# Optimization experiments

Measured on AMD Instinct MI355X. Metric: run time of the kernel, lower is better.

The kernel has to match this reference:

```python
import jax, jax.numpy as jnp
import numpy as np

V, H, L = 32000, 512, 1
B, S = 16, 64


def setup_inputs() -> dict:
    key = jax.random.key(0)
    ks = jax.random.split(key, 10)
    inp = {
        "target_seqs": jax.random.randint(ks[0], (B, S), 0, V),
        "thought": jax.random.normal(ks[1], (1, B, H), dtype=jnp.float32),
        "hidden": jax.random.normal(ks[2], (L, B, H), dtype=jnp.float32),
        # parameters
        "emb": jax.random.normal(ks[3], (V, H), dtype=jnp.float32) * 0.02,
        "W_ih": jax.random.normal(ks[4], (3 * H, 2 * H), dtype=jnp.float32) * (1.0 / np.sqrt(H)),
        "W_hh": jax.random.normal(ks[5], (3 * H, H), dtype=jnp.float32) * (1.0 / np.sqrt(H)),
        "b_ih": jax.random.normal(ks[6], (3 * H,), dtype=jnp.float32) * 0.01,
        "b_hh": jax.random.normal(ks[7], (3 * H,), dtype=jnp.float32) * 0.01,
        "W_out": jax.random.normal(ks[8], (V, H), dtype=jnp.float32) * (1.0 / np.sqrt(H)),
        "b_out": jax.random.normal(ks[9], (V,), dtype=jnp.float32) * 0.01,
    }
    return inp


def gru_layer(x_sbd, h0, W_ih, W_hh, b_ih, b_hh):
    # x_sbd: [S,B,2H]; h0: [B,H]. Torch GRU cell math.
    # Precompute input projections for all timesteps: [S,B,3H]
    gi = jnp.einsum('sbd,gd->sbg', x_sbd, W_ih) + b_ih

    def step(h, gi_t):
        gh = h @ W_hh.T + b_hh                       # [B,3H]
        i_r, i_z, i_n = jnp.split(gi_t, 3, axis=-1)
        h_r, h_z, h_n = jnp.split(gh, 3, axis=-1)
        r = jax.nn.sigmoid(i_r + h_r)
        z = jax.nn.sigmoid(i_z + h_z)
        n = jnp.tanh(i_n + r * h_n)
        h_new = (1.0 - z) * n + z * h
        return h_new, h_new

    h_last, ys = jax.lax.scan(step, h0, gi)
    return ys, h_last                                 # [S,B,H], [B,H]


def reference(target_seqs, thought, hidden, emb, W_ih, W_hh, b_ih, b_hh, W_out, b_out):
    embedded = emb[target_seqs]                        # [B,S,H]
    # fused broadcast-concat replacing the python double loop
    th = jnp.broadcast_to(thought[0][:, None, :], embedded.shape)  # [B,S,H]
    rnn_input = jnp.concatenate([embedded, th], axis=-1)           # [B,S,2H]
    x_sbd = jnp.transpose(rnn_input, (1, 0, 2))                    # [S,B,2H]
    ys, h_last = gru_layer(x_sbd, hidden[0], W_ih, W_hh, b_ih, b_hh)
    output = jnp.transpose(ys, (1, 0, 2))              # [B,S,H]
    logits = jnp.einsum('bsh,vh->bsv', output, W_out) + b_out
    logp = jax.nn.log_softmax(logits, axis=-1)         # [B,S,V]
    return logp, h_last[None]                          # hidden: [1,B,H]
```

## Files before the change

### kernel.cpp

```cpp
#include <hip/hip_runtime.h>

typedef unsigned int u32;
typedef unsigned short u16;
typedef short s16x8 __attribute__((ext_vector_type(8)));
typedef float f32x4 __attribute__((ext_vector_type(4)));

#define SENT 0xFFFFFFFFu

__device__ __forceinline__ u16 f2bf(float f) {
  u32 u = __float_as_uint(f);
  u32 r = (u + 0x7fffu + ((u >> 16) & 1u)) >> 16;
  return (u16)r;
}

__device__ __forceinline__ uint4 load_u4_bypass(const u32* p) {
  uint4 r;
  asm volatile("global_load_dwordx4 %0, %1, off sc0 sc1\n\ts_waitcnt vmcnt(0)"
               : "=v"(r) : "v"(p) : "memory");
  return r;
}

__device__ __forceinline__ void gload16(const u16* g, u16* l) {
  __builtin_amdgcn_global_load_lds(
      (const __attribute__((address_space(1))) unsigned int*)(g),
      (__attribute__((address_space(3))) unsigned int*)(l), 16, 0, 0);
}

__global__ __launch_bounds__(256) void cvt_bf16_kernel(const float* __restrict__ src,
                                                       u16* __restrict__ dst, int n4) {
  int i = blockIdx.x * 256 + threadIdx.x;
  if (i >= n4) return;
  float4 v = reinterpret_cast<const float4*>(src)[i];
  u32 lo = (u32)f2bf(v.x) | ((u32)f2bf(v.y) << 16);
  u32 hi = (u32)f2bf(v.z) | ((u32)f2bf(v.w) << 16);
  reinterpret_cast<uint2*>(dst)[i] = make_uint2(lo, hi);
}

__global__ __launch_bounds__(128) void build_x_kernel(const int* __restrict__ tseq,
                                                      const float* __restrict__ emb,
                                                      const float* __restrict__ thought,
                                                      u16* __restrict__ x) {
  int m = blockIdx.x;
  int s = m >> 4, b = m & 15;
  int tid = threadIdx.x;
  int k = tid * 8;
  const float* src;
  if (k < 512) src = emb + (size_t)tseq[b * 64 + s] * 512 + k;
  else         src = thought + b * 512 + (k - 512);
  float4 v0 = reinterpret_cast<const float4*>(src)[0];
  float4 v1 = reinterpret_cast<const float4*>(src)[1];
  uint4 o;
  o.x = (u32)f2bf(v0.x) | ((u32)f2bf(v0.y) << 16);
  o.y = (u32)f2bf(v0.z) | ((u32)f2bf(v0.w) << 16);
  o.z = (u32)f2bf(v1.x) | ((u32)f2bf(v1.y) << 16);
  o.w = (u32)f2bf(v1.z) | ((u32)f2bf(v1.w) << 16);
  *reinterpret_cast<uint4*>(x + (size_t)m * 1024 + k) = o;
}

template <bool LSE>
__global__ __launch_bounds__(256) void gemm_bt_kernel(const u16* __restrict__ A,
                                                      const u16* __restrict__ Bm,
                                                      const float* __restrict__ bias,
                                                      float* __restrict__ C,
                                                      int M_, int N_, int K_,
                                                      float* __restrict__ partials, int nnb) {
  __shared__ u16 sA[2][4096];
  __shared__ u16 sB[2][4096];
  __shared__ float pm[2][128];
  __shared__ float ps[2][128];
  int nb = blockIdx.x, mb = blockIdx.y;
  int m0 = mb * 128, n0 = nb * 128;
  int tid = threadIdx.x;
  int wave = tid >> 6, lane = tid & 63;
  int wm = wave >> 1, wn = wave & 1;
  int l16 = lane & 15, quad = lane >> 4;
  int c0 = wave * 128 + lane, c1 = c0 + 64;
  int r0 = c0 >> 2, co0 = (c0 & 3) * 8;
  int r1 = c1 >> 2, co1 = (c1 & 3) * 8;
  const u16* gA0 = A + (size_t)(m0 + r0) * K_ + co0;
  const u16* gA1 = A + (size_t)(m0 + r1) * K_ + co1;
  const u16* gB0 = Bm + (size_t)(n0 + r0) * K_ + co0;
  const u16* gB1 = Bm + (size_t)(n0 + r1) * K_ + co1;
  int wbase = wave * 1024;

  auto STAGE = [&](int buf, int k0) {
    gload16(gA0 + k0, &sA[buf][wbase]);
    gload16(gA1 + k0, &sA[buf][wbase + 512]);
    gload16(gB0 + k0, &sB[buf][wbase]);
    gload16(gB1 + k0, &sB[buf][wbase + 512]);
  };

  f32x4 acc[4][4];
  for (int i = 0; i < 4; ++i)
    for (int j = 0; j < 4; ++j) acc[i][j] = (f32x4){0.f, 0.f, 0.f, 0.f};

  int NK = K_ >> 5;
  STAGE(0, 0);
  __syncthreads();
  int cur = 0;
  for (int ks = 0; ks < NK; ++ks) {
    if (ks + 1 < NK) STAGE(cur ^ 1, (ks + 1) * 32);
    s16x8 af[4], bfr[4];
    for (int mt = 0; mt < 4; ++mt)
      af[mt] = *reinterpret_cast<const s16x8*>(&sA[cur][(wm * 64 + mt * 16 + l16) * 32 + quad * 8]);
    for (int nt = 0; nt < 4; ++nt)
      bfr[nt] = *reinterpret_cast<const s16x8*>(&sB[cur][(wn * 64 + nt * 16 + l16) * 32 + quad * 8]);
    for (int mt = 0; mt < 4; ++mt)
      for (int nt = 0; nt < 4; ++nt)
        acc[mt][nt] = __builtin_amdgcn_mfma_f32_16x16x32_bf16(af[mt], bfr[nt], acc[mt][nt], 0, 0, 0);
    if (ks + 1 < NK) {
      __syncthreads();
      cur ^= 1;
    }
  }

  int rbase = wm * 64 + quad * 4;
  int cbase = n0 + wn * 64 + l16;
  for (int nt = 0; nt < 4; ++nt) {
    float bv = bias[cbase + nt * 16];
    for (int mt = 0; mt < 4; ++mt)
      for (int r = 0; r < 4; ++r) acc[mt][nt][r] += bv;
  }
  for (int mt = 0; mt < 4; ++mt)
    for (int r = 0; r < 4; ++r) {
      int row = m0 + rbase + mt * 16 + r;
      for (int nt = 0; nt < 4; ++nt)
        C[(size_t)row * N_ + cbase + nt * 16] = acc[mt][nt][r];
    }
  if (LSE) {
    for (int mt = 0; mt < 4; ++mt)
      for (int r = 0; r < 4; ++r) {
        float mx = acc[mt][0][r];
        for (int nt = 1; nt < 4; ++nt) mx = fmaxf(mx, acc[mt][nt][r]);
        for (int d = 1; d < 16; d <<= 1) mx = fmaxf(mx, __shfl_xor(mx, d));
        float sm = 0.f;
        for (int nt = 0; nt < 4; ++nt) sm += __expf(acc[mt][nt][r] - mx);
        for (int d = 1; d < 16; d <<= 1) sm += __shfl_xor(sm, d);
        if (l16 == 0) {
          int rr = wm * 64 + mt * 16 + quad * 4 + r;
          pm[wn][rr] = mx;
          ps[wn][rr] = sm;
        }
      }
    __syncthreads();
    if (tid < 128) {
      float m1 = pm[0][tid], m2 = pm[1][tid];
      float s1 = ps[0][tid], s2 = ps[1][tid];
      float Mx = fmaxf(m1, m2);
      float Sx = s1 * __expf(m1 - Mx) + s2 * __expf(m2 - Mx);
      float* p = partials + ((size_t)(m0 + tid) * nnb + nb) * 2;
      p[0] = Mx;
      p[1] = Sx;
    }
  }
}

__global__ __launch_bounds__(256, 2) void gru_kernel(const float* __restrict__ gi,
                                                     const float* __restrict__ W_hh,
                                                     const float* __restrict__ b_hh,
                                                     const float* __restrict__ hidden,
                                                     u32* __restrict__ hbase,
                                                     u16* __restrict__ ys,
                                                     float* __restrict__ hlast,
                                                     const float* __restrict__ wout_f32,
                                                     u16* __restrict__ wout_bf) {
  __shared__ u16 sW[48 * 520];
  __shared__ float h_s[576];
  int wg = blockIdx.x;
  int tid = threadIdx.x;

  if (wg >= 512) {
    for (int i = (wg - 512) * 256 + tid; i < 4096000; i += 256 * 256) {
      float4 v = reinterpret_cast<const float4*>(wout_f32)[i];
      u32 lo = (u32)f2bf(v.x) | ((u32)f2bf(v.y) << 16);
      u32 hi = (u32)f2bf(v.z) | ((u32)f2bf(v.w) << 16);
      reinterpret_cast<uint2*>(wout_bf)[i] = make_uint2(lo, hi);
    }
    return;
  }

  int b = wg >> 5, g = wg & 31;
  for (int e = tid * 4; e < 48 * 512; e += 1024) {
    int lr = e >> 9, col = e & 511;
    int grow = (lr >> 4) * 512 + g * 16 + (lr & 15);
    float4 v = *reinterpret_cast<const float4*>(W_hh + (size_t)grow * 512 + col);
    u32 lo = (u32)f2bf(v.x) | ((u32)f2bf(v.y) << 16);
    u32 hi = (u32)f2bf(v.z) | ((u32)f2bf(v.w) << 16);
    *reinterpret_cast<uint2*>(&sW[lr * 520 + col]) = make_uint2(lo, hi);
  }
  int grp = tid >> 4, l16 = tid & 15;
  int j = g * 16 + grp;
  float bhr = 0.f, bhz = 0.f, bhn = 0.f;
  if (l16 == 0) { bhr = b_hh[j]; bhz = b_hh[512 + j]; bhn = b_hh[1024 + j]; }
  int j0 = tid * 4;
  if (tid < 128) {
    float4 f = *reinterpret_cast<const float4*>(hidden + b * 512 + j0);
    *reinterpret_cast<float4*>(&h_s[j0 + ((j0 >> 5) << 2)]) = f;
  }
  __syncthreads();

  for (int t = 0; t < 64; ++t) {
    float gir = 0.f, giz = 0.f, gin = 0.f;
    if (l16 == 0) {
      size_t gib = ((size_t)t * 16 + b) * 1536;
      gir = gi[gib + j]; giz = gi[gib + 512 + j]; gin = gi[gib + 1024 + j];
    }
    if (t > 0) {
      const u32* hp = hbase + (size_t)(t - 1) * 8192 + b * 512;
      if (tid < 32) {
        const u32* fp = hp + tid * 16;
        u32 v = __hip_atomic_load(fp, __ATOMIC_RELAXED, __HIP_MEMORY_SCOPE_AGENT);
        while (v == SENT) {
          __builtin_amdgcn_s_sleep(2);
          v = __hip_atomic_load(fp, __ATOMIC_RELAXED, __HIP_MEMORY_SCOPE_AGENT);
        }
      }
      __syncthreads();
      if (tid < 128) {
        uint4 v = load_u4_bypass(hp + j0);
        while (v.x == SENT || v.y == SENT || v.z == SENT || v.w == SENT) {
          __builtin_amdgcn_s_sleep(1);
          v = load_u4_bypass(hp + j0);
        }
        float4 f;
        f.x = __uint_as_float(v.x); f.y = __uint_as_float(v.y);
        f.z = __uint_as_float(v.z); f.w = __uint_as_float(v.w);
        *reinterpret_cast<float4*>(&h_s[j0 + ((j0 >> 5) << 2)]) = f;
      }
      __syncthreads();
    }
    float hreg[32];
    int hb2 = l16 * 36;
    for (int c4 = 0; c4 < 4; ++c4) {
      float4 x0 = *reinterpret_cast<const float4*>(&h_s[hb2 + c4 * 8]);
      float4 x1 = *reinterpret_cast<const float4*>(&h_s[hb2 + c4 * 8 + 4]);
      hreg[c4 * 8 + 0] = x0.x; hreg[c4 * 8 + 1] = x0.y;
      hreg[c4 * 8 + 2] = x0.z; hreg[c4 * 8 + 3] = x0.w;
      hreg[c4 * 8 + 4] = x1.x; hreg[c4 * 8 + 5] = x1.y;
      hreg[c4 * 8 + 6] = x1.z; hreg[c4 * 8 + 7] = x1.w;
    }
    float a0 = 0.f, a1 = 0.f, a2 = 0.f;
    const u16* wr0 = &sW[grp * 520 + l16 * 32];
    const u16* wr1 = wr0 + 16 * 520;
    const u16* wr2 = wr0 + 32 * 520;
    for (int c4 = 0; c4 < 4; ++c4) {
      uint4 w0 = *reinterpret_cast<const uint4*>(wr0 + c4 * 8);
      uint4 w1 = *reinterpret_cast<const uint4*>(wr1 + c4 * 8);
      uint4 w2 = *reinterpret_cast<const uint4*>(wr2 + c4 * 8);
      const float* hh = &hreg[c4 * 8];
      a0 += __uint_as_float(w0.x << 16) * hh[0] + __uint_as_float(w0.x & 0xffff0000u) * hh[1];
      a0 += __uint_as_float(w0.y << 16) * hh[2] + __uint_as_float(w0.y & 0xffff0000u) * hh[3];
      a0 += __uint_as_float(w0.z << 16) * hh[4] + __uint_as_float(w0.z & 0xffff0000u) * hh[5];
      a0 += __uint_as_float(w0.w << 16) * hh[6] + __uint_as_float(w0.w & 0xffff0000u) * hh[7];
      a1 += __uint_as_float(w1.x << 16) * hh[0] + __uint_as_float(w1.x & 0xffff0000u) * hh[1];
      a1 += __uint_as_float(w1.y << 16) * hh[2] + __uint_as_float(w1.y & 0xffff0000u) * hh[3];
      a1 += __uint_as_float(w1.z << 16) * hh[4] + __uint_as_float(w1.z & 0xffff0000u) * hh[5];
      a1 += __uint_as_float(w1.w << 16) * hh[6] + __uint_as_float(w1.w & 0xffff0000u) * hh[7];
      a2 += __uint_as_float(w2.x << 16) * hh[0] + __uint_as_float(w2.x & 0xffff0000u) * hh[1];
      a2 += __uint_as_float(w2.y << 16) * hh[2] + __uint_as_float(w2.y & 0xffff0000u) * hh[3];
      a2 += __uint_as_float(w2.z << 16) * hh[4] + __uint_as_float(w2.z & 0xffff0000u) * hh[5];
      a2 += __uint_as_float(w2.w << 16) * hh[6] + __uint_as_float(w2.w & 0xffff0000u) * hh[7];
    }
    for (int d = 1; d < 16; d <<= 1) {
      a0 += __shfl_xor(a0, d);
      a1 += __shfl_xor(a1, d);
      a2 += __shfl_xor(a2, d);
    }
    if (l16 == 0) {
      float er = __expf(-(gir + a0 + bhr));
      float ez = __expf(-(giz + a1 + bhz));
      float r = __fdividef(1.f, 1.f + er);
      float z = __fdividef(1.f, 1.f + ez);
      float xn = gin + r * (a2 + bhn);
      float en = __expf(2.f * xn);
      float n = 1.f - __fdividef(2.f, en + 1.f);
      float hprev = h_s[j + ((j >> 5) << 2)];
      float hv = (1.f - z) * n + z * hprev;
      __hip_atomic_store(hbase + (size_t)t * 8192 + b * 512 + j, __float_as_uint(hv),
                         __ATOMIC_RELAXED, __HIP_MEMORY_SCOPE_AGENT);
      ys[((size_t)b * 64 + t) * 512 + j] = f2bf(hv);
      if (t == 63) hlast[b * 512 + j] = hv;
    }
  }
}

__global__ __launch_bounds__(64) void lse_combine_kernel(const float* __restrict__ partials,
                                                         float* __restrict__ lse, int nnb) {
  int row = blockIdx.x;
  int lane = threadIdx.x;
  float M = -INFINITY, S = 0.f;
  for (int i = lane; i < nnb; i += 64) {
    const float* p = partials + ((size_t)row * nnb + i) * 2;
    float m2 = p[0], s2 = p[1];
    if (m2 > M) { float tt = M; M = m2; m2 = tt; tt = S; S = s2; s2 = tt; }
    if (s2 > 0.f) S += s2 * __expf(m2 - M);
  }
  for (int d = 1; d < 64; d <<= 1) {
    float m2 = __shfl_xor(M, d), s2 = __shfl_xor(S, d);
    if (m2 > M) { float tt = M; M = m2; m2 = tt; tt = S; S = s2; s2 = tt; }
    if (s2 > 0.f) S += s2 * __expf(m2 - M);
  }
  if (lane == 0) lse[row] = M + logf(S);
}

__global__ __launch_bounds__(256) void sub_lse_kernel(float* __restrict__ out,
                                                      const float* __restrict__ lse) {
  int i = blockIdx.x * 256 + threadIdx.x;
  int row = i / 8000;
  float l = lse[row];
  float4 v = reinterpret_cast<float4*>(out)[i];
  v.x -= l; v.y -= l; v.z -= l; v.w -= l;
  reinterpret_cast<float4*>(out)[i] = v;
}

extern "C" void kernel_launch(void* const* d_in, const int* in_sizes, int n_in,
                              void* d_out, int out_size, void* d_ws, size_t ws_size,
                              hipStream_t stream) {
  const int* tseq = (const int*)d_in[0];
  const float* thought = (const float*)d_in[1];
  const float* hidden = (const float*)d_in[2];
  const float* emb = (const float*)d_in[3];
  const float* W_ih = (const float*)d_in[4];
  const float* W_hh = (const float*)d_in[5];
  const float* b_ih = (const float*)d_in[6];
  const float* b_hh = (const float*)d_in[7];
  const float* W_out = (const float*)d_in[8];
  const float* b_out = (const float*)d_in[9];
  float* out = (float*)d_out;

  char* ws = (char*)d_ws;
  size_t off = 0;
  auto alloc = [&](size_t bytes) {
    void* p = ws + off;
    off = (off + bytes + 255) & ~(size_t)255;
    return p;
  };
  u16* wout_bf = (u16*)alloc((size_t)32000 * 512 * 2);
  u16* wih_bf  = (u16*)alloc((size_t)1536 * 1024 * 2);
  u16* x_bf    = (u16*)alloc((size_t)1024 * 1024 * 2);
  u16* ys_bf   = (u16*)alloc((size_t)1024 * 512 * 2);
  float* gi    = (float*)alloc((size_t)1024 * 1536 * 4);
  u32* hbase   = (u32*)alloc((size_t)64 * 16 * 512 * 4);
  float* partials = (float*)alloc((size_t)1024 * 250 * 2 * 4);
  float* lse   = (float*)alloc((size_t)1024 * 4);
  (void)ws_size; (void)in_sizes; (void)n_in; (void)out_size;

  hipMemsetAsync(hbase, 0xFF, (size_t)64 * 16 * 512 * 4, stream);
  cvt_bf16_kernel<<<1536, 256, 0, stream>>>(W_ih, wih_bf, 393216);
  build_x_kernel<<<1024, 128, 0, stream>>>(tseq, emb, thought, x_bf);
  gemm_bt_kernel<false><<<dim3(12, 8), 256, 0, stream>>>(x_bf, wih_bf, b_ih, gi,
                                                         1024, 1536, 1024, nullptr, 0);
  gru_kernel<<<768, 256, 0, stream>>>(gi, W_hh, b_hh, hidden, hbase, ys_bf,
                                      out + 32768000, W_out, wout_bf);
  gemm_bt_kernel<true><<<dim3(250, 8), 256, 0, stream>>>(ys_bf, wout_bf, b_out, out,
                                                         1024, 32000, 512, partials, 250);
  lse_combine_kernel<<<1024, 64, 0, stream>>>(partials, lse, 250);
  sub_lse_kernel<<<32000, 256, 0, stream>>>(out, lse);
}
```

Measured before the change: 473.2 us.

## Fuse prep kernels, remap GEMM block order across XCDs, merge LSE combine and subtract

Merges the W_ih conversion, input gather and hbase sentinel memset into a single pre_kernel. Switches both GEMMs to a 1D grid whose block index is remapped so the 8 M-blocks sharing an N-tile land together, improving L2 reuse of the weight tiles across XCDs. Fuses the LSE partial combine with the in-place log-prob subtraction, one block per row, which removes two launches and the separate lse buffer. The per-row combined kernel has less parallelism per block, which may cost bandwidth on the large output pass.

```diff
diff --git a/kernel.cpp b/kernel.cpp
--- a/kernel.cpp
+++ b/kernel.cpp
@@ -26,35 +26,34 @@
       (__attribute__((address_space(3))) unsigned int*)(l), 16, 0, 0);
 }
 
-__global__ __launch_bounds__(256) void cvt_bf16_kernel(const float* __restrict__ src,
-                                                       u16* __restrict__ dst, int n4) {
-  int i = blockIdx.x * 256 + threadIdx.x;
-  if (i >= n4) return;
-  float4 v = reinterpret_cast<const float4*>(src)[i];
-  u32 lo = (u32)f2bf(v.x) | ((u32)f2bf(v.y) << 16);
-  u32 hi = (u32)f2bf(v.z) | ((u32)f2bf(v.w) << 16);
-  reinterpret_cast<uint2*>(dst)[i] = make_uint2(lo, hi);
-}
-
-__global__ __launch_bounds__(128) void build_x_kernel(const int* __restrict__ tseq,
-                                                      const float* __restrict__ emb,
-                                                      const float* __restrict__ thought,
-                                                      u16* __restrict__ x) {
-  int m = blockIdx.x;
-  int s = m >> 4, b = m & 15;
-  int tid = threadIdx.x;
-  int k = tid * 8;
-  const float* src;
-  if (k < 512) src = emb + (size_t)tseq[b * 64 + s] * 512 + k;
-  else         src = thought + b * 512 + (k - 512);
-  float4 v0 = reinterpret_cast<const float4*>(src)[0];
-  float4 v1 = reinterpret_cast<const float4*>(src)[1];
-  uint4 o;
-  o.x = (u32)f2bf(v0.x) | ((u32)f2bf(v0.y) << 16);
-  o.y = (u32)f2bf(v0.z) | ((u32)f2bf(v0.w) << 16);
-  o.z = (u32)f2bf(v1.x) | ((u32)f2bf(v1.y) << 16);
-  o.w = (u32)f2bf(v1.z) | ((u32)f2bf(v1.w) << 16);
-  *reinterpret_cast<uint4*>(x + (size_t)m * 1024 + k) = o;
+__global__ __launch_bounds__(256) void pre_kernel(const float* __restrict__ W_ih,
+                                                  u16* __restrict__ wih_bf,
+                                                  const int* __restrict__ tseq,
+                                                  const float* __restrict__ emb,
+                                                  const float* __restrict__ thought,
+                                                  u16* __restrict__ x,
+                                                  u32* __restrict__ hbase) {
+  int blk = blockIdx.x, tid = threadIdx.x;
+  if (blk < 1536) {
+    int i = blk * 256 + tid;
+    float4 v = reinterpret_cast<const float4*>(W_ih)[i];
+    u32 lo = (u32)f2bf(v.x) | ((u32)f2bf(v.y) << 16);
+    u32 hi = (u32)f2bf(v.z) | ((u32)f2bf(v.w) << 16);
+    reinterpret_cast<uint2*>(wih_bf)[i] = make_uint2(lo, hi);
+  } else if (blk < 2560) {
+    int m = blk - 1536;
+    int s = m >> 4, b = m & 15;
+    int k = tid * 4;
+    const float* src = (k < 512) ? emb + (size_t)tseq[b * 64 + s] * 512 + k
+                                 : thought + b * 512 + (k - 512);
+    float4 v = *reinterpret_cast<const float4*>(src);
+    *reinterpret_cast<uint2*>(x + (size_t)m * 1024 + k) =
+        make_uint2((u32)f2bf(v.x) | ((u32)f2bf(v.y) << 16),
+                   (u32)f2bf(v.z) | ((u32)f2bf(v.w) << 16));
+  } else {
+    int i = (blk - 2560) * 256 + tid;
+    reinterpret_cast<uint4*>(hbase)[i] = make_uint4(SENT, SENT, SENT, SENT);
+  }
 }
 
 template <bool LSE>
@@ -68,7 +67,10 @@
   __shared__ u16 sB[2][4096];
   __shared__ float pm[2][128];
   __shared__ float ps[2][128];
-  int nb = blockIdx.x, mb = blockIdx.y;
+  int bid = blockIdx.x;
+  int nwg8 = gridDim.x >> 3;
+  int wgid = (bid & 7) * nwg8 + (bid >> 3);
+  int mb = wgid & 7, nb = wgid >> 3;
   int m0 = mb * 128, n0 = nb * 128;
   int tid = threadIdx.x;
   int wave = tid >> 6, lane = tid & 63;
@@ -284,33 +286,37 @@
   }
 }
 
-__global__ __launch_bounds__(64) void lse_combine_kernel(const float* __restrict__ partials,
-                                                         float* __restrict__ lse, int nnb) {
+__global__ __launch_bounds__(256) void lse_sub_kernel(const float* __restrict__ partials,
+                                                      float* __restrict__ out, int nnb) {
+  __shared__ float sM[4], sS[4];
   int row = blockIdx.x;
-  int lane = threadIdx.x;
+  int tid = threadIdx.x;
+  int lane = tid & 63, wv = tid >> 6;
   float M = -INFINITY, S = 0.f;
-  for (int i = lane; i < nnb; i += 64) {
-    const float* p = partials + ((size_t)row * nnb + i) * 2;
-    float m2 = p[0], s2 = p[1];
-    if (m2 > M) { float tt = M; M = m2; m2 = tt; tt = S; S = s2; s2 = tt; }
-    if (s2 > 0.f) S += s2 * __expf(m2 - M);
+  if (tid < nnb) {
+    const float* p = partials + ((size_t)row * nnb + tid) * 2;
+    M = p[0]; S = p[1];
   }
   for (int d = 1; d < 64; d <<= 1) {
     float m2 = __shfl_xor(M, d), s2 = __shfl_xor(S, d);
     if (m2 > M) { float tt = M; M = m2; m2 = tt; tt = S; S = s2; s2 = tt; }
     if (s2 > 0.f) S += s2 * __expf(m2 - M);
   }
-  if (lane == 0) lse[row] = M + logf(S);
-}
-
-__global__ __launch_bounds__(256) void sub_lse_kernel(float* __restrict__ out,
-                                                      const float* __restrict__ lse) {
-  int i = blockIdx.x * 256 + threadIdx.x;
-  int row = i / 8000;
-  float l = lse[row];
-  float4 v = reinterpret_cast<float4*>(out)[i];
-  v.x -= l; v.y -= l; v.z -= l; v.w -= l;
-  reinterpret_cast<float4*>(out)[i] = v;
+  if (lane == 0) { sM[wv] = M; sS[wv] = S; }
+  __syncthreads();
+  M = sM[0]; S = sS[0];
+  for (int w = 1; w < 4; ++w) {
+    float m2 = sM[w], s2 = sS[w];
+    if (m2 > M) { float tt = M; M = m2; m2 = tt; tt = S; S = s2; s2 = tt; }
+    if (s2 > 0.f) S += s2 * __expf(m2 - M);
+  }
+  float l = M + logf(S);
+  float4* po = reinterpret_cast<float4*>(out + (size_t)row * 32000);
+  for (int i = tid; i < 8000; i += 256) {
+    float4 v = po[i];
+    v.x -= l; v.y -= l; v.z -= l; v.w -= l;
+    po[i] = v;
+  }
 }
 
 extern "C" void kernel_launch(void* const* d_in, const int* in_sizes, int n_in,
@@ -342,18 +348,14 @@
   float* gi    = (float*)alloc((size_t)1024 * 1536 * 4);
   u32* hbase   = (u32*)alloc((size_t)64 * 16 * 512 * 4);
   float* partials = (float*)alloc((size_t)1024 * 250 * 2 * 4);
-  float* lse   = (float*)alloc((size_t)1024 * 4);
   (void)ws_size; (void)in_sizes; (void)n_in; (void)out_size;
 
-  hipMemsetAsync(hbase, 0xFF, (size_t)64 * 16 * 512 * 4, stream);
-  cvt_bf16_kernel<<<1536, 256, 0, stream>>>(W_ih, wih_bf, 393216);
-  build_x_kernel<<<1024, 128, 0, stream>>>(tseq, emb, thought, x_bf);
-  gemm_bt_kernel<false><<<dim3(12, 8), 256, 0, stream>>>(x_bf, wih_bf, b_ih, gi,
-                                                         1024, 1536, 1024, nullptr, 0);
+  pre_kernel<<<3072, 256, 0, stream>>>(W_ih, wih_bf, tseq, emb, thought, x_bf, hbase);
+  gemm_bt_kernel<false><<<96, 256, 0, stream>>>(x_bf, wih_bf, b_ih, gi,
+                                                1024, 1536, 1024, nullptr, 0);
   gru_kernel<<<768, 256, 0, stream>>>(gi, W_hh, b_hh, hidden, hbase, ys_bf,
                                       out + 32768000, W_out, wout_bf);
-  gemm_bt_kernel<true><<<dim3(250, 8), 256, 0, stream>>>(ys_bf, wout_bf, b_out, out,
-                                                         1024, 32000, 512, partials, 250);
-  lse_combine_kernel<<<1024, 64, 0, stream>>>(partials, lse, 250);
-  sub_lse_kernel<<<32000, 256, 0, stream>>>(out, lse);
-}
+  gemm_bt_kernel<true><<<2000, 256, 0, stream>>>(ys_bf, wout_bf, b_out, out,
+                                                 1024, 32000, 512, partials, 250);
+  lse_sub_kernel<<<1024, 256, 0, stream>>>(partials, out, 250);
+}
```

Measured after the change: 460.9 us. 2.6% less time.
